# Performance work log

Measured on AMD Instinct MI355X. Metric: run time of the kernel, lower is better.

## Reference

```python
import math
import jax, jax.numpy as jnp
import numpy as np

EMBED_DIM = 1024
NUM_HEADS = 16
HEAD_DIM = EMBED_DIM // NUM_HEADS


def setup_inputs() -> dict:
    key = jax.random.key(0)
    k1, k2, k3, k4 = jax.random.split(key, 4)
    B, S = 4, 2048
    x = jax.random.normal(k1, (B, S, EMBED_DIM), dtype=jnp.float32)
    mask = jnp.ones((B, S), dtype=jnp.int32)  # key-padding mask, 1 = keep
    # nn.Linear(embed_dim, 3*embed_dim, bias=False): weight [3E, E]
    w_qkv = jax.random.normal(k2, (3 * EMBED_DIM, EMBED_DIM), dtype=jnp.float32) / math.sqrt(EMBED_DIM)
    # nn.Linear(embed_dim, embed_dim): weight [E, E], bias [E]
    w_out = jax.random.normal(k3, (EMBED_DIM, EMBED_DIM), dtype=jnp.float32) / math.sqrt(EMBED_DIM)
    b_out = jax.random.normal(k4, (EMBED_DIM,), dtype=jnp.float32) * 0.01
    return {"x": x, "w_qkv": w_qkv, "w_out": w_out, "b_out": b_out, "mask": mask}


def _attention(x, w_qkv, w_out, b_out, mask):
    B, S, E = x.shape
    qkv = jnp.einsum("bse,fe->bsf", x, w_qkv)  # [B,S,3E]
    q, k, v = jnp.split(qkv, 3, axis=-1)
    def heads(t):  # [B,S,E] -> [B,H,S,D]
        return t.reshape(B, S, NUM_HEADS, HEAD_DIM).transpose(0, 2, 1, 3)
    q, k, v = heads(q), heads(k), heads(v)
    scores = jnp.einsum("bhqd,bhkd->bhqk", q, k) / math.sqrt(HEAD_DIM)
    keep = (mask != 0)[:, None, None, :]  # [B,1,1,S]
    scores = jnp.where(keep, scores, jnp.float32(-1e9))
    probs = jax.nn.softmax(scores, axis=-1)
    # dropout p=0.0 -> identity (eval semantics)
    out = jnp.einsum("bhqk,bhkd->bhqd", probs, v)
    out = out.transpose(0, 2, 1, 3).reshape(B, S, E)
    return jnp.einsum("bse,fe->bsf", out, w_out) + b_out


def reference(x, w_qkv, w_out, b_out, mask):
    return _attention(x, w_qkv, w_out, b_out, mask)
```

## Files before the change

kernel.cpp:

```cpp
#include <hip/hip_runtime.h>

#define EMB 1024
#define NH 16
#define HD 64
#define SEQ 2048
#define BB 4

typedef __attribute__((ext_vector_type(8))) short bf8;
typedef __attribute__((ext_vector_type(4))) short bf4;
typedef __attribute__((ext_vector_type(4))) float f4;

#define MFMA16(a, b, c) __builtin_amdgcn_mfma_f32_16x16x32_bf16((a), (b), (c), 0, 0, 0)

#if defined(__has_builtin)
#if __has_builtin(__builtin_amdgcn_mfma_f32_16x16x16_bf16_1k)
#define HAVE_MFMA16X16 1
#endif
#endif

__device__ inline f4 pv_mfma(bf4 a, bf4 b, f4 c) {
#ifdef HAVE_MFMA16X16
  return __builtin_amdgcn_mfma_f32_16x16x16_bf16_1k(a, b, c, 0, 0, 0);
#else
  bf8 av, bv;
  *(bf4*)&av = a;  ((int*)&av)[2] = 0; ((int*)&av)[3] = 0;
  *(bf4*)&bv = b;  ((int*)&bv)[2] = 0; ((int*)&bv)[3] = 0;
  return __builtin_amdgcn_mfma_f32_16x16x32_bf16(av, bv, c, 0, 0, 0);
#endif
}

#define GLL16(g, l)                                                     \
  __builtin_amdgcn_global_load_lds(                                     \
      (__attribute__((address_space(1))) void*)(g),                     \
      (__attribute__((address_space(3))) void*)(l), 16, 0, 0)

__device__ inline unsigned short f2bf(float f) {
  union { float f; unsigned u; } v; v.f = f;
  unsigned u = v.u;
  u += 0x7fffu + ((u >> 16) & 1u);
  return (unsigned short)(u >> 16);
}

__device__ inline unsigned pkbf(float a, float b) {
  union { float f; unsigned u; } ua, ub; ua.f = a; ub.f = b;
  return ((ua.u + 0x8000u) >> 16) | ((ub.u + 0x8000u) & 0xFFFF0000u);
}

__global__ void cvt_f32_bf16(const float* __restrict__ in,
                             unsigned short* __restrict__ out, int n4) {
  int i = blockIdx.x * blockDim.x + threadIdx.x;
  if (i < n4) {
    float4 f = ((const float4*)in)[i];
    ushort4 o;
    o.x = f2bf(f.x); o.y = f2bf(f.y); o.z = f2bf(f.z); o.w = f2bf(f.w);
    ((ushort4*)out)[i] = o;
  }
}

template <bool OUTF32>
__global__ __launch_bounds__(256, 2) void gemm_bt(
    const unsigned short* __restrict__ A, const unsigned short* __restrict__ B,
    void* __restrict__ Cout, const float* __restrict__ bias,
    unsigned short* __restrict__ vtb,
    int M, int N, int K, int ldC, int nsplit) {
  __shared__ unsigned short la[128 * 32];
  __shared__ unsigned short lb[128 * 32];

  const int t = threadIdx.x;
  const int lane = t & 63;
  const int w = t >> 6;
  const int quad = lane >> 4;
  const int lcol = lane & 15;
  const int m0 = blockIdx.y * 128;
  const int n0 = blockIdx.x * 128;
  const int wm = (w & 1) * 64;
  const int wn = (w >> 1) * 64;

  f4 acc[4][4];
#pragma unroll
  for (int i = 0; i < 4; i++)
#pragma unroll
    for (int j = 0; j < 4; j++) acc[i][j] = (f4){0.f, 0.f, 0.f, 0.f};

  const int srow = t >> 2;
  const int scol = (t & 3) * 8;
  const unsigned short* gA = A + (size_t)(m0 + srow) * K + scol;
  const unsigned short* gB = B + (size_t)(n0 + srow) * K + scol;
  unsigned short* lA = la + t * 8;
  unsigned short* lB = lb + t * 8;

  for (int kt = 0; kt < K; kt += 32) {
    __syncthreads();
    GLL16(gA + kt, lA);
    GLL16(gA + kt + (size_t)64 * K, lA + 64 * 32);
    GLL16(gB + kt, lB);
    GLL16(gB + kt + (size_t)64 * K, lB + 64 * 32);
    __syncthreads();

    bf8 af[4], bfr[4];
#pragma unroll
    for (int i = 0; i < 4; i++) {
      af[i]  = *(const bf8*)&la[(wm + i * 16 + lcol) * 32 + quad * 8];
      bfr[i] = *(const bf8*)&lb[(wn + i * 16 + lcol) * 32 + quad * 8];
    }
#pragma unroll
    for (int i = 0; i < 4; i++)
#pragma unroll
      for (int j = 0; j < 4; j++)
        acc[i][j] = MFMA16(af[i], bfr[j], acc[i][j]);
  }

  if (!OUTF32 && n0 >= nsplit) {
#pragma unroll
    for (int i = 0; i < 4; i++) {
#pragma unroll
      for (int j = 0; j < 4; j++) {
        int f = n0 + wn + j * 16 + lcol - nsplit;
        int mg = m0 + wm + i * 16 + quad * 4;
        int bb = mg >> 11, ss = mg & 2047;
        ushort4 pk;
        pk.x = f2bf(acc[i][j][0]); pk.y = f2bf(acc[i][j][1]);
        pk.z = f2bf(acc[i][j][2]); pk.w = f2bf(acc[i][j][3]);
        *(ushort4*)&vtb[((size_t)(bb * 1024 + f)) * 2048 + ss] = pk;
      }
    }
  } else {
#pragma unroll
    for (int i = 0; i < 4; i++) {
#pragma unroll
      for (int j = 0; j < 4; j++) {
#pragma unroll
        for (int r = 0; r < 4; r++) {
          int m = m0 + wm + i * 16 + quad * 4 + r;
          int n = n0 + wn + j * 16 + lcol;
          if (OUTF32) {
            float v = acc[i][j][r] + (bias ? bias[n] : 0.f);
            ((float*)Cout)[(size_t)m * ldC + n] = v;
          } else {
            ((unsigned short*)Cout)[(size_t)m * ldC + n] = f2bf(acc[i][j][r]);
          }
        }
      }
    }
  }
}

#define LSTR 72
#define SCALE_LOG2E 0.1803368801111244f

__global__ __launch_bounds__(256, 4) void attn_kernel(
    const unsigned short* __restrict__ qk, const unsigned short* __restrict__ vtg,
    const int* __restrict__ mask, unsigned short* __restrict__ outb) {
  __shared__ unsigned short kt[64 * LSTR];
  __shared__ unsigned short vt[64 * LSTR];
  __shared__ __align__(16) float bt[64];

  const int t = threadIdx.x;
  const int lane = t & 63;
  const int w = t >> 6;
  const int quad = lane >> 4;
  const int lcol = lane & 15;
  const int q0 = blockIdx.x * 64;
  const int h = blockIdx.y;
  const int b = blockIdx.z;

  const unsigned short* qbase = qk + (size_t)(b * SEQ) * 2048 + h * HD;
  const unsigned short* kbase = qbase + 1024;
  const unsigned short* vbase = vtg + (size_t)((b * 16 + h) * 64) * SEQ;

  const int qrow = q0 + w * 16 + lcol;
  const bf8 qf0 = *(const bf8*)(qbase + (size_t)qrow * 2048 + quad * 8);
  const bf8 qf1 = *(const bf8*)(qbase + (size_t)qrow * 2048 + 32 + quad * 8);

  f4 o[4];
#pragma unroll
  for (int db = 0; db < 4; db++) o[db] = (f4){0.f, 0.f, 0.f, 0.f};
  float m_i = -1e30f, l_i = 0.f;

  const int sr = t >> 2;
  const int sc = (t & 3) * 16;
  const unsigned short* gk = kbase + (size_t)sr * 2048 + sc;
  const unsigned short* gv = vbase + (size_t)sr * SEQ + sc;

  uint4 pk0 = *(const uint4*)gk;
  uint4 pk1 = *(const uint4*)(gk + 8);
  uint4 pv0 = *(const uint4*)gv;
  uint4 pv1 = *(const uint4*)(gv + 8);
  int pmv = (t < 64) ? mask[b * SEQ + t] : 0;

  for (int k0 = 0; k0 < SEQ; k0 += 64) {
    __syncthreads();
    *(uint4*)&kt[sr * LSTR + sc] = pk0;
    *(uint4*)&kt[sr * LSTR + sc + 8] = pk1;
    *(uint4*)&vt[sr * LSTR + sc] = pv0;
    *(uint4*)&vt[sr * LSTR + sc + 8] = pv1;
    if (t < 64) bt[t] = pmv ? 0.f : -1e30f;
    __syncthreads();

    {
      int kn = (k0 + 64 < SEQ) ? k0 + 64 : k0;
      pk0 = *(const uint4*)(gk + (size_t)kn * 2048);
      pk1 = *(const uint4*)(gk + (size_t)kn * 2048 + 8);
      pv0 = *(const uint4*)(gv + kn);
      pv1 = *(const uint4*)(gv + kn + 8);
      pmv = (t < 64) ? mask[b * SEQ + kn + t] : 0;
    }

    f4 sT[4];
#pragma unroll
    for (int kb = 0; kb < 4; kb++) {
      bf8 kf0 = *(const bf8*)&kt[(kb * 16 + lcol) * LSTR + quad * 8];
      bf8 kf1 = *(const bf8*)&kt[(kb * 16 + lcol) * LSTR + 32 + quad * 8];
      f4 a = (f4){0.f, 0.f, 0.f, 0.f};
      a = MFMA16(kf0, qf0, a);
      a = MFMA16(kf1, qf1, a);
      sT[kb] = a;
    }

    float pv[4][4];
    float mt = -1e30f;
#pragma unroll
    for (int kb = 0; kb < 4; kb++) {
      float4 bb = *(const float4*)&bt[kb * 16 + quad * 4];
      pv[kb][0] = fmaf(sT[kb][0], SCALE_LOG2E, bb.x);
      pv[kb][1] = fmaf(sT[kb][1], SCALE_LOG2E, bb.y);
      pv[kb][2] = fmaf(sT[kb][2], SCALE_LOG2E, bb.z);
      pv[kb][3] = fmaf(sT[kb][3], SCALE_LOG2E, bb.w);
#pragma unroll
      for (int r = 0; r < 4; r++) mt = fmaxf(mt, pv[kb][r]);
    }
    mt = fmaxf(mt, __shfl_xor(mt, 16));
    mt = fmaxf(mt, __shfl_xor(mt, 32));

    float mnew = fmaxf(m_i, mt);
    float alpha = exp2f(m_i - mnew);
    float rsum = 0.f;
#pragma unroll
    for (int kb = 0; kb < 4; kb++)
#pragma unroll
      for (int r = 0; r < 4; r++) {
        float e = exp2f(pv[kb][r] - mnew);
        pv[kb][r] = e;
        rsum += e;
      }
    rsum += __shfl_xor(rsum, 16);
    rsum += __shfl_xor(rsum, 32);
    l_i = l_i * alpha + rsum;
    m_i = mnew;

    bf4 pfrag[4];
#pragma unroll
    for (int kb = 0; kb < 4; kb++) {
      unsigned u0 = pkbf(pv[kb][0], pv[kb][1]);
      unsigned u1 = pkbf(pv[kb][2], pv[kb][3]);
      union { unsigned u[2]; bf4 s; } cv;
      cv.u[0] = u0; cv.u[1] = u1;
      pfrag[kb] = cv.s;
    }

#pragma unroll
    for (int db = 0; db < 4; db++)
#pragma unroll
      for (int r = 0; r < 4; r++) o[db][r] *= alpha;

#pragma unroll
    for (int db = 0; db < 4; db++) {
#pragma unroll
      for (int kb = 0; kb < 4; kb++) {
        bf4 vf = *(const bf4*)&vt[(db * 16 + lcol) * LSTR + kb * 16 + quad * 4];
        o[db] = pv_mfma(vf, pfrag[kb], o[db]);
      }
    }
  }

  float inv = 1.f / l_i;
#pragma unroll
  for (int db = 0; db < 4; db++) {
    ushort4 pk;
    pk.x = f2bf(o[db][0] * inv);
    pk.y = f2bf(o[db][1] * inv);
    pk.z = f2bf(o[db][2] * inv);
    pk.w = f2bf(o[db][3] * inv);
    *(ushort4*)&outb[(size_t)(b * SEQ + q0 + w * 16 + lcol) * EMB + h * HD +
                     db * 16 + quad * 4] = pk;
  }
}

extern "C" void kernel_launch(void* const* d_in, const int* in_sizes, int n_in,
                              void* d_out, int out_size, void* d_ws, size_t ws_size,
                              hipStream_t stream) {
  const float* x     = (const float*)d_in[0];
  const float* w_qkv = (const float*)d_in[1];
  const float* w_out = (const float*)d_in[2];
  const float* b_out = (const float*)d_in[3];
  const int*   mask  = (const int*)d_in[4];

  char* ws = (char*)d_ws;
  unsigned short* xb    = (unsigned short*)(ws + 0);
  unsigned short* wqkvb = (unsigned short*)(ws + 16777216);
  unsigned short* woutb = (unsigned short*)(ws + 23068672);
  unsigned short* qkb   = (unsigned short*)(ws + 25165824);
  unsigned short* attnb = (unsigned short*)(ws + 58720256);
  unsigned short* vtb   = (unsigned short*)(ws + 75497472);

  cvt_f32_bf16<<<8192, 256, 0, stream>>>(x, xb, 8388608 / 4);
  cvt_f32_bf16<<<3072, 256, 0, stream>>>(w_qkv, wqkvb, 3145728 / 4);
  cvt_f32_bf16<<<1024, 256, 0, stream>>>(w_out, woutb, 1048576 / 4);

  gemm_bt<false><<<dim3(24, 64), 256, 0, stream>>>(
      xb, wqkvb, (void*)qkb, nullptr, vtb, 8192, 3072, 1024, 2048, 2048);

  attn_kernel<<<dim3(32, 16, 4), 256, 0, stream>>>(qkb, vtb, mask, attnb);

  gemm_bt<true><<<dim3(8, 64), 256, 0, stream>>>(
      attnb, woutb, d_out, b_out, nullptr, 8192, 1024, 1024, 1024, 1 << 30);
}
```

Baseline: 364.7 us.

## Load K/V tiles via global_load_lds with XOR-swizzled unpadded LDS layout

Replaces the register-prefetched K/V tile loads and padded LDS stores with direct global-to-LDS loads into an XOR-swizzled 64x64 layout, and adjusts the fragment reads to match. It also skips the online-softmax rescale when no row max increases, uses the hardware exp2 builtin, and raises the launch-bounds occupancy hint from 4 to 6. The intent is to cut VGPR pressure and LDS bank conflicts and to raise occupancy. The cost is that the register prefetch overlap of the next tile is lost, since the global load now sits between the two barriers.

```diff
diff --git a/kernel.cpp b/kernel.cpp
--- a/kernel.cpp
+++ b/kernel.cpp
@@ -16,6 +16,12 @@
 #if __has_builtin(__builtin_amdgcn_mfma_f32_16x16x16_bf16_1k)
 #define HAVE_MFMA16X16 1
 #endif
+#if __has_builtin(__builtin_amdgcn_exp2f)
+#define EXP2F __builtin_amdgcn_exp2f
+#endif
+#endif
+#ifndef EXP2F
+#define EXP2F exp2f
 #endif
 
 __device__ inline f4 pv_mfma(bf4 a, bf4 b, f4 c) {
@@ -145,14 +151,13 @@
   }
 }
 
-#define LSTR 72
 #define SCALE_LOG2E 0.1803368801111244f
 
-__global__ __launch_bounds__(256, 4) void attn_kernel(
+__global__ __launch_bounds__(256, 6) void attn_kernel(
     const unsigned short* __restrict__ qk, const unsigned short* __restrict__ vtg,
     const int* __restrict__ mask, unsigned short* __restrict__ outb) {
-  __shared__ unsigned short kt[64 * LSTR];
-  __shared__ unsigned short vt[64 * LSTR];
+  __shared__ unsigned short kt[64 * 64];
+  __shared__ unsigned short vt[64 * 64];
   __shared__ __align__(16) float bt[64];
 
   const int t = threadIdx.x;
@@ -160,6 +165,7 @@
   const int w = t >> 6;
   const int quad = lane >> 4;
   const int lcol = lane & 15;
+  const int lx = lcol & 7;
   const int q0 = blockIdx.x * 64;
   const int h = blockIdx.y;
   const int b = blockIdx.z;
@@ -177,40 +183,35 @@
   for (int db = 0; db < 4; db++) o[db] = (f4){0.f, 0.f, 0.f, 0.f};
   float m_i = -1e30f, l_i = 0.f;
 
-  const int sr = t >> 2;
-  const int sc = (t & 3) * 16;
+  const int sr = t >> 3;
+  const int sc = ((t & 7) ^ (sr & 7)) * 8;
   const unsigned short* gk = kbase + (size_t)sr * 2048 + sc;
   const unsigned short* gv = vbase + (size_t)sr * SEQ + sc;
-
-  uint4 pk0 = *(const uint4*)gk;
-  uint4 pk1 = *(const uint4*)(gk + 8);
-  uint4 pv0 = *(const uint4*)gv;
-  uint4 pv1 = *(const uint4*)(gv + 8);
+  unsigned short* lk = kt + t * 8;
+  unsigned short* lv = vt + t * 8;
+
   int pmv = (t < 64) ? mask[b * SEQ + t] : 0;
 
   for (int k0 = 0; k0 < SEQ; k0 += 64) {
     __syncthreads();
-    *(uint4*)&kt[sr * LSTR + sc] = pk0;
-    *(uint4*)&kt[sr * LSTR + sc + 8] = pk1;
-    *(uint4*)&vt[sr * LSTR + sc] = pv0;
-    *(uint4*)&vt[sr * LSTR + sc + 8] = pv1;
+    GLL16(gk + (size_t)k0 * 2048, lk);
+    GLL16(gk + (size_t)(k0 + 32) * 2048, lk + 2048);
+    GLL16(gv + k0, lv);
+    GLL16(gv + k0 + 32 * SEQ, lv + 2048);
     if (t < 64) bt[t] = pmv ? 0.f : -1e30f;
     __syncthreads();
 
     {
-      int kn = (k0 + 64 < SEQ) ? k0 + 64 : k0;
-      pk0 = *(const uint4*)(gk + (size_t)kn * 2048);
-      pk1 = *(const uint4*)(gk + (size_t)kn * 2048 + 8);
-      pv0 = *(const uint4*)(gv + kn);
-      pv1 = *(const uint4*)(gv + kn + 8);
+      int kn = (k0 + 64 < SEQ) ? k0 + 64 : 0;
       pmv = (t < 64) ? mask[b * SEQ + kn + t] : 0;
     }
 
     f4 sT[4];
 #pragma unroll
     for (int kb = 0; kb < 4; kb++) {
-      bf8 kf0 = *(const bf8*)&kt[(kb * 16 + lcol) * LSTR + quad * 8];
-      bf8 kf1 = *(const bf8*)&kt[(kb * 16 + lcol) * LSTR + 32 + quad * 8];
+      const unsigned short* krow = kt + (kb * 16 + lcol) * 64;
+      bf8 kf0 = *(const bf8*)&krow[(quad ^ lx) * 8];
+      bf8 kf1 = *(const bf8*)&krow[((4 + quad) ^ lx) * 8];
       f4 a = (f4){0.f, 0.f, 0.f, 0.f};
       a = MFMA16(kf0, qf0, a);
       a = MFMA16(kf1, qf1, a);
@@ -233,41 +234,45 @@
     mt = fmaxf(mt, __shfl_xor(mt, 32));
 
     float mnew = fmaxf(m_i, mt);
-    float alpha = exp2f(m_i - mnew);
+    if (__any(mnew > m_i)) {
+      float alpha = EXP2F(m_i - mnew);
+      l_i *= alpha;
+#pragma unroll
+      for (int db = 0; db < 4; db++)
+#pragma unroll
+        for (int r = 0; r < 4; r++) o[db][r] *= alpha;
+      m_i = mnew;
+    }
+
     float rsum = 0.f;
 #pragma unroll
     for (int kb = 0; kb < 4; kb++)
 #pragma unroll
       for (int r = 0; r < 4; r++) {
-        float e = exp2f(pv[kb][r] - mnew);
+        float e = EXP2F(pv[kb][r] - m_i);
         pv[kb][r] = e;
         rsum += e;
       }
     rsum += __shfl_xor(rsum, 16);
     rsum += __shfl_xor(rsum, 32);
-    l_i = l_i * alpha + rsum;
-    m_i = mnew;
+    l_i += rsum;
 
     bf4 pfrag[4];
 #pragma unroll
     for (int kb = 0; kb < 4; kb++) {
-      unsigned u0 = pkbf(pv[kb][0], pv[kb][1]);
-      unsigned u1 = pkbf(pv[kb][2], pv[kb][3]);
       union { unsigned u[2]; bf4 s; } cv;
-      cv.u[0] = u0; cv.u[1] = u1;
+      cv.u[0] = pkbf(pv[kb][0], pv[kb][1]);
+      cv.u[1] = pkbf(pv[kb][2], pv[kb][3]);
       pfrag[kb] = cv.s;
     }
 
 #pragma unroll
-    for (int db = 0; db < 4; db++)
-#pragma unroll
-      for (int r = 0; r < 4; r++) o[db][r] *= alpha;
-
-#pragma unroll
     for (int db = 0; db < 4; db++) {
+      const unsigned short* vrow = vt + (db * 16 + lcol) * 64;
 #pragma unroll
       for (int kb = 0; kb < 4; kb++) {
-        bf4 vf = *(const bf4*)&vt[(db * 16 + lcol) * LSTR + kb * 16 + quad * 4];
+        bf4 vf = *(const bf4*)&vrow[(((kb << 1) | (quad >> 1)) ^ lx) * 8 +
+                                    (quad & 1) * 4];
         o[db] = pv_mfma(vf, pfrag[kb], o[db]);
       }
     }
```

After: 345.5 us. -5.3%, faster.
